# Kernel tuning notes

Hardware: AMD Instinct MI355X
Metric: run time of the kernel (lower is better)

The kernel has to match this reference:

```python
import jax, jax.numpy as jnp
import numpy as np
import math

D = 1024      # d_model
H = 16        # n_heads
DH = 64       # d_head
V = 32000     # vocab_size
MAXS = 2048   # max_seq_length
B, S = 2, 2048
PAD = 0
NEG = -1000000000.0
EPS = 1e-5


def _layernorm(x, g, b):
    mu = jnp.mean(x, axis=-1, keepdims=True)
    var = jnp.mean(jnp.square(x - mu), axis=-1, keepdims=True)
    return (x - mu) * jax.lax.rsqrt(var + EPS) * g + b


def _pad_mask(ids):
    # (b,1,1,S) additive mask over key columns where token == PAD
    return jnp.where((ids == PAD)[:, None, None, :], NEG, 0.0).astype(jnp.float32)


def _attn(Q, K, V_, out_w, out_b, causal_mask, pad_mask):
    # Q,K,V_: [b,n,s,d]
    logits = jnp.einsum('bnqd,bnkd->bnqk', Q, K) / math.sqrt(DH)
    if causal_mask is not None:
        logits = logits + causal_mask
    if pad_mask is not None:
        logits = logits + pad_mask
    probs = jax.nn.softmax(logits, axis=-1)
    o = jnp.einsum('bnqk,bnkd->bnqd', probs, V_)
    b, n, s, d = o.shape
    o = o.transpose(0, 2, 1, 3).reshape(b, s, n * d)  # b s (n d)
    return o @ out_w + out_b


def _heads(x, w, b):
    y = x @ w + b  # [b,s,H*DH]
    bs, s, _ = y.shape
    return y.reshape(bs, s, H, DH).transpose(0, 2, 1, 3)  # b n s d


def setup_inputs() -> dict:
    key = jax.random.key(0)
    ks = jax.random.split(key, 32)
    p = lambda i, shp, sc=0.02: (jax.random.normal(ks[i], shp, jnp.float32) * sc)
    inp = {
        'input_embedding': jax.random.normal(ks[0], (B, S, D), jnp.float32),
        'input_ids': jax.random.randint(ks[1], (B, S), 0, V),
        'target_ids': jax.random.randint(ks[2], (B, S), 0, V),
        'tok_emb': p(3, (V, D), 1.0),
        'pos_emb': p(4, (MAXS, D), 1.0),
        'ln1_g': jnp.ones((D,)), 'ln1_b': jnp.zeros((D,)),
        'q1_w': p(5, (D, H * DH)), 'q1_b': jnp.zeros((H * DH,)),
        'k1_w': p(6, (D, H * DH)), 'k1_b': jnp.zeros((H * DH,)),
        'v1_w': p(7, (D, H * DH)), 'v1_b': jnp.zeros((H * DH,)),
        'out1_w': p(8, (H * DH, D)), 'out1_b': jnp.zeros((D,)),
        'ln2_g': jnp.ones((D,)), 'ln2_b': jnp.zeros((D,)),
        'q2_w': p(9, (D, H * DH)), 'q2_b': jnp.zeros((H * DH,)),
        'k2_w': p(10, (D, H * DH)), 'k2_b': jnp.zeros((H * DH,)),
        'v2_w': p(11, (D, H * DH)), 'v2_b': jnp.zeros((H * DH,)),
        'out2_w': p(12, (H * DH, D)), 'out2_b': jnp.zeros((D,)),
        'ln3_g': jnp.ones((D,)), 'ln3_b': jnp.zeros((D,)),
        'mlp_w1': p(13, (D, 4 * D)), 'mlp_b1': jnp.zeros((4 * D,)),
        'mlp_w2': p(14, (4 * D, D)), 'mlp_b2': jnp.zeros((D,)),
    }
    return inp


def reference(input_embedding, input_ids, target_ids, tok_emb, pos_emb,
              ln1_g, ln1_b, q1_w, q1_b, k1_w, k1_b, v1_w, v1_b, out1_w, out1_b,
              ln2_g, ln2_b, q2_w, q2_b, k2_w, k2_b, v2_w, v2_b, out2_w, out2_b,
              ln3_g, ln3_b, mlp_w1, mlp_b1, mlp_w2, mlp_b2):
    b, s = target_ids.shape
    # embedding + positional
    x = tok_emb[target_ids] + pos_emb[jnp.arange(s)][None, :, :]
    x = _layernorm(x, ln1_g, ln1_b)
    # masked self-attention
    Q = _heads(x, q1_w, q1_b)
    K = _heads(x, k1_w, k1_b)
    Vv = _heads(x, v1_w, v1_b)
    causal = jnp.triu(jnp.full((s, s), NEG, jnp.float32), k=1)[None, None]
    attn = _attn(Q, K, Vv, out1_w, out1_b, causal, _pad_mask(target_ids))
    h = x + attn
    h = _layernorm(h, ln2_g, ln2_b)
    # cross-attention against encoder states
    Qc = _heads(h, q2_w, q2_b)
    Kc = _heads(input_embedding, k2_w, k2_b)
    Vc = _heads(input_embedding, v2_w, v2_b)
    cross = _attn(Qc, Kc, Vc, out2_w, out2_b, None, _pad_mask(input_ids))
    r = cross + h
    # MLP with exact GELU (torch nn.GELU default)
    z = _layernorm(r, ln3_g, ln3_b)
    mlp = jax.nn.gelu(z @ mlp_w1 + mlp_b1, approximate=False) @ mlp_w2 + mlp_b2
    return mlp + r
```

## Files before the change

kernel.cpp:

```cpp
#include <hip/hip_runtime.h>
#include <hip/hip_bf16.h>

#define S_LEN 2048
#define NEGF -1000000000.0f
#define QSC 0.18033688f

typedef unsigned short ushort_t;
typedef __attribute__((ext_vector_type(8))) short short8;
typedef __attribute__((ext_vector_type(4))) float f32x4;

#if defined(__has_builtin)
#if __has_builtin(__builtin_amdgcn_exp2f)
#define EXP2 __builtin_amdgcn_exp2f
#endif
#endif
#ifndef EXP2
#define EXP2 exp2f
#endif

__device__ __forceinline__ unsigned short f2b(float f) {
  unsigned int u = __float_as_uint(f);
  return (unsigned short)((u + 0x7fffu + ((u >> 16) & 1u)) >> 16);
}

__device__ __forceinline__ void gld_lds16(const void* g, void* l) {
  __builtin_amdgcn_global_load_lds((__attribute__((address_space(1))) unsigned int*)g,
                                   (__attribute__((address_space(3))) unsigned int*)l, 16, 0, 0);
}

__device__ __forceinline__ void wtrans_body(const float* __restrict__ W,
                                            ushort_t* __restrict__ Wt, int K, int N,
                                            int bx, int by) {
  __shared__ float t[32][33];
  int n0 = bx * 32, k0 = by * 32;
  int tx = threadIdx.x & 31, ty = threadIdx.x >> 5;
#pragma unroll
  for (int i = 0; i < 32; i += 8)
    t[ty + i][tx] = W[(size_t)(k0 + ty + i) * N + n0 + tx];
  __syncthreads();
#pragma unroll
  for (int i = 0; i < 32; i += 8)
    Wt[(size_t)(n0 + ty + i) * K + k0 + tx] = f2b(t[tx][ty + i]);
}

__global__ __launch_bounds__(256) void wtrans(const float* __restrict__ W,
                                              ushort_t* __restrict__ Wt, int K, int N) {
  wtrans_body(W, Wt, K, N, blockIdx.x, blockIdx.y);
}

struct P8 {
  const float* s[8];
  ushort_t* d[8];
};
__global__ __launch_bounds__(256) void wtrans8(P8 p) {
  wtrans_body(p.s[blockIdx.z], p.d[blockIdx.z], 1024, 1024, blockIdx.x, blockIdx.y);
}

__global__ __launch_bounds__(256) void f2bcvt(const float* __restrict__ in,
                                              ushort_t* __restrict__ out) {
  size_t i = ((size_t)blockIdx.x * 256 + threadIdx.x) * 4;
  float4 v = *(const float4*)(in + i);
  union { unsigned short u[4]; uint2 q; } pk;
  pk.u[0] = f2b(v.x); pk.u[1] = f2b(v.y); pk.u[2] = f2b(v.z); pk.u[3] = f2b(v.w);
  *(uint2*)(out + i) = pk.q;
}

__global__ __launch_bounds__(256) void bcat(float* __restrict__ dst, const float* __restrict__ a,
                                            const float* __restrict__ b,
                                            const float* __restrict__ c, int n0, int n1) {
  int i = blockIdx.x * 256 + threadIdx.x;
  float v = (i < n0) ? a[i] : (i < n0 + n1 ? b[i - n0] : c[i - n0 - n1]);
  dst[i] = v;
}

__global__ __launch_bounds__(256) void padmask(const int* __restrict__ tids,
                                               const int* __restrict__ iids,
                                               float* __restrict__ pmA,
                                               float* __restrict__ pmB) {
  int i = blockIdx.x * 256 + threadIdx.x;
  pmA[i] = (tids[i] == 0) ? NEGF : 0.0f;
  pmB[i] = (iids[i] == 0) ? NEGF : 0.0f;
}

__device__ __forceinline__ void row_stats(float s, float ss, float* outMean, float* outRstd) {
  __shared__ float red[8];
#pragma unroll
  for (int o = 32; o > 0; o >>= 1) {
    s += __shfl_down(s, o);
    ss += __shfl_down(ss, o);
  }
  int wave = threadIdx.x >> 6, lane = threadIdx.x & 63;
  if (lane == 0) { red[wave] = s; red[4 + wave] = ss; }
  __syncthreads();
  if (threadIdx.x == 0) {
    float S0 = red[0] + red[1] + red[2] + red[3];
    float S1 = red[4] + red[5] + red[6] + red[7];
    float mean = S0 * (1.0f / 1024.0f);
    float var = S1 * (1.0f / 1024.0f) - mean * mean;
    red[0] = mean;
    red[1] = rsqrtf(var + 1e-5f);
  }
  __syncthreads();
  *outMean = red[0];
  *outRstd = red[1];
}

__global__ __launch_bounds__(256) void embed_ln(const int* __restrict__ tids,
                                                const float* __restrict__ tok,
                                                const float* __restrict__ pos,
                                                const float* __restrict__ g,
                                                const float* __restrict__ be,
                                                float* __restrict__ xf,
                                                ushort_t* __restrict__ xb) {
  int row = blockIdx.x;
  int s = row & (S_LEN - 1);
  int id = tids[row];
  int c = threadIdx.x * 4;
  float4 v = *(const float4*)(tok + (size_t)id * 1024 + c);
  float4 p = *(const float4*)(pos + (size_t)s * 1024 + c);
  v.x += p.x; v.y += p.y; v.z += p.z; v.w += p.w;
  float mean, rstd;
  row_stats(v.x + v.y + v.z + v.w, v.x * v.x + v.y * v.y + v.z * v.z + v.w * v.w, &mean, &rstd);
  float4 gv = *(const float4*)(g + c);
  float4 bv = *(const float4*)(be + c);
  float4 o;
  o.x = (v.x - mean) * rstd * gv.x + bv.x;
  o.y = (v.y - mean) * rstd * gv.y + bv.y;
  o.z = (v.z - mean) * rstd * gv.z + bv.z;
  o.w = (v.w - mean) * rstd * gv.w + bv.w;
  *(float4*)(xf + (size_t)row * 1024 + c) = o;
  union { unsigned short u[4]; uint2 q; } pk;
  pk.u[0] = f2b(o.x); pk.u[1] = f2b(o.y); pk.u[2] = f2b(o.z); pk.u[3] = f2b(o.w);
  *(uint2*)(xb + (size_t)row * 1024 + c) = pk.q;
}

__global__ __launch_bounds__(256) void ln_fwd(const float* in, const float* __restrict__ g,
                                              const float* __restrict__ be, float* outF,
                                              ushort_t* __restrict__ outB) {
  int row = blockIdx.x;
  int c = threadIdx.x * 4;
  float4 v = *(const float4*)(in + (size_t)row * 1024 + c);
  float mean, rstd;
  row_stats(v.x + v.y + v.z + v.w, v.x * v.x + v.y * v.y + v.z * v.z + v.w * v.w, &mean, &rstd);
  float4 gv = *(const float4*)(g + c);
  float4 bv = *(const float4*)(be + c);
  float4 o;
  o.x = (v.x - mean) * rstd * gv.x + bv.x;
  o.y = (v.y - mean) * rstd * gv.y + bv.y;
  o.z = (v.z - mean) * rstd * gv.z + bv.z;
  o.w = (v.w - mean) * rstd * gv.w + bv.w;
  if (outF) *(float4*)(outF + (size_t)row * 1024 + c) = o;
  union { unsigned short u[4]; uint2 q; } pk;
  pk.u[0] = f2b(o.x); pk.u[1] = f2b(o.y); pk.u[2] = f2b(o.z); pk.u[3] = f2b(o.w);
  *(uint2*)(outB + (size_t)row * 1024 + c) = pk.q;
}

__global__ __launch_bounds__(256) void gemm_bt(const ushort_t* __restrict__ A,
                                               const ushort_t* __restrict__ Bt,
                                               const float* __restrict__ bias,
                                               const float* __restrict__ res,
                                               float* __restrict__ outF,
                                               ushort_t* __restrict__ outB,
                                               ushort_t* __restrict__ outT,
                                               int M, int N, int K, int act, int scaleN,
                                               int nSplit) {
  __shared__ __align__(16) ushort_t lA[128 * 64];
  __shared__ __align__(16) ushort_t lB[128 * 64];
  const int tid = threadIdx.x;
  const int wave = tid >> 6, lane = tid & 63;
  const int quad = lane >> 4, l16 = lane & 15;
  const int m0 = blockIdx.y * 128, n0 = blockIdx.x * 128;
  const int wm = (wave >> 1) * 64, wn = (wave & 1) * 64;

  f32x4 zero4 = {0.f, 0.f, 0.f, 0.f};
  f32x4 acc[4][4];
#pragma unroll
  for (int i = 0; i < 4; ++i)
#pragma unroll
    for (int j = 0; j < 4; ++j) acc[i][j] = zero4;

  int rowS[4], chkS[4];
#pragma unroll
  for (int ii = 0; ii < 4; ++ii) {
    int d = (wave * 4 + ii) * 64 + lane;
    rowS[ii] = d >> 3;
    chkS[ii] = (d & 7) ^ (rowS[ii] & 7);
  }

  for (int kt = 0; kt < K; kt += 64) {
    __syncthreads();
#pragma unroll
    for (int ii = 0; ii < 4; ++ii) {
      gld_lds16(A + (size_t)(m0 + rowS[ii]) * K + kt + chkS[ii] * 8,
                (char*)lA + (wave * 4 + ii) * 1024);
      gld_lds16(Bt + (size_t)(n0 + rowS[ii]) * K + kt + chkS[ii] * 8,
                (char*)lB + (wave * 4 + ii) * 1024);
    }
    __syncthreads();
#pragma unroll
    for (int kc = 0; kc < 2; ++kc) {
      short8 af[4], bf[4];
#pragma unroll
      for (int mt = 0; mt < 4; ++mt) {
        int r = wm + mt * 16 + l16;
        int c = (kc * 4 + quad) ^ (r & 7);
        af[mt] = *(const short8*)(lA + r * 64 + c * 8);
      }
#pragma unroll
      for (int nt = 0; nt < 4; ++nt) {
        int r = wn + nt * 16 + l16;
        int c = (kc * 4 + quad) ^ (r & 7);
        bf[nt] = *(const short8*)(lB + r * 64 + c * 8);
      }
#pragma unroll
      for (int mt = 0; mt < 4; ++mt)
#pragma unroll
        for (int nt = 0; nt < 4; ++nt)
          acc[mt][nt] = __builtin_amdgcn_mfma_f32_16x16x32_bf16(af[mt], bf[nt], acc[mt][nt], 0, 0, 0);
    }
  }

#pragma unroll
  for (int nt = 0; nt < 4; ++nt) {
    int gn = n0 + wn + nt * 16 + l16;
    float bv = bias[gn];
    if (gn < nSplit) {
#pragma unroll
      for (int mt = 0; mt < 4; ++mt) {
        int gmb = m0 + wm + mt * 16 + quad * 4;
#pragma unroll
        for (int reg = 0; reg < 4; ++reg) {
          size_t idx = (size_t)(gmb + reg) * nSplit + gn;
          float v = acc[mt][nt][reg] + bv;
          if (act == 1) v = 0.5f * v * (1.0f + erff(v * 0.70710678118654752f));
          if (gn < scaleN) v *= QSC;
          if (res) v += res[idx];
          if (outF) outF[idx] = v;
          if (outB) outB[idx] = f2b(v);
        }
      }
    } else {
#pragma unroll
      for (int mt = 0; mt < 4; ++mt) {
        int gmb = m0 + wm + mt * 16 + quad * 4;
        union { unsigned short u[4]; uint2 q; } pk;
#pragma unroll
        for (int reg = 0; reg < 4; ++reg) pk.u[reg] = f2b(acc[mt][nt][reg] + bv);
        *(uint2*)(outT + (size_t)(gn - nSplit) * M + gmb) = pk.q;
      }
    }
  }
}

__global__ __launch_bounds__(512, 2) void gemm256(const ushort_t* __restrict__ A,
                                                  const ushort_t* __restrict__ Bt,
                                                  const float* __restrict__ bias,
                                                  const float* __restrict__ res,
                                                  float* __restrict__ outF,
                                                  ushort_t* __restrict__ outB,
                                                  ushort_t* __restrict__ outT,
                                                  int M, int N, int K, int act, int scaleN,
                                                  int nSplit) {
  __shared__ __align__(16) ushort_t sA[2][256 * 64];
  __shared__ __align__(16) ushort_t sB[2][256 * 64];
  const int tid = threadIdx.x;
  const int wave = tid >> 6, lane = tid & 63;
  const int quad = lane >> 4, l16 = lane & 15;
  const int m0 = blockIdx.y * 256, n0 = blockIdx.x * 256;
  const int wm = (wave >> 2) * 128, wn = (wave & 3) * 64;

  const ushort_t* Ab = A + (size_t)m0 * K;
  const ushort_t* Bb = Bt + (size_t)n0 * K;

  const int srow = tid >> 3;
  const int schk = ((tid & 7) ^ (srow & 7)) << 3;

#define STAGE_H(SRC, LD, KT, DST, H)                                          \
  do {                                                                        \
    gld_lds16((SRC) + (size_t)((H) * 128 + srow) * (LD) + (KT) + schk,        \
              (char*)(DST) + (H) * 16384 + tid * 16);                         \
    gld_lds16((SRC) + (size_t)((H) * 128 + 64 + srow) * (LD) + (KT) + schk,   \
              (char*)(DST) + (H) * 16384 + 8192 + tid * 16);                  \
  } while (0)

  f32x4 zero4 = {0.f, 0.f, 0.f, 0.f};
  f32x4 acc[8][4];
#pragma unroll
  for (int i = 0; i < 8; ++i)
#pragma unroll
    for (int j = 0; j < 4; ++j) acc[i][j] = zero4;

  const int NT = K >> 6;

  STAGE_H(Ab, K, 0, sA[0], 0);
  STAGE_H(Ab, K, 0, sA[0], 1);
  STAGE_H(Bb, K, 0, sB[0], 0);
  STAGE_H(Bb, K, 0, sB[0], 1);
  asm volatile("s_waitcnt vmcnt(0)" ::: "memory");
  __builtin_amdgcn_s_barrier();

  for (int t = 0; t < NT; ++t) {
    const ushort_t* curA = sA[t & 1];
    const ushort_t* curB = sB[t & 1];
    ushort_t* nxtA = sA[(t + 1) & 1];
    ushort_t* nxtB = sB[(t + 1) & 1];
    const int ktn = (t + 1) << 6;
    const bool more = (t + 1 < NT);
#pragma unroll
    for (int q = 0; q < 4; ++q) {
      const int mh = q >> 1, nh = q & 1;
      short8 af[4][2], bf[2][2];
#pragma unroll
      for (int mt = 0; mt < 4; ++mt)
#pragma unroll
        for (int kc = 0; kc < 2; ++kc) {
          int r = wm + (mh * 4 + mt) * 16 + l16;
          af[mt][kc] = *(const short8*)(curA + r * 64 + (((kc * 4 + quad) ^ (r & 7)) << 3));
        }
#pragma unroll
      for (int nt = 0; nt < 2; ++nt)
#pragma unroll
        for (int kc = 0; kc < 2; ++kc) {
          int r = wn + (nh * 2 + nt) * 16 + l16;
          bf[nt][kc] = *(const short8*)(curB + r * 64 + (((kc * 4 + quad) ^ (r & 7)) << 3));
        }
      if (more) {
        if (q == 0) {
          STAGE_H(Ab, K, ktn, nxtA, 0);
          STAGE_H(Ab, K, ktn, nxtA, 1);
        } else if (q == 1) {
          STAGE_H(Bb, K, ktn, nxtB, 0);
          STAGE_H(Bb, K, ktn, nxtB, 1);
        }
      }
      __builtin_amdgcn_s_barrier();
      asm volatile("s_waitcnt lgkmcnt(0)" ::: "memory");
      __builtin_amdgcn_s_setprio(1);
#pragma unroll
      for (int mt = 0; mt < 4; ++mt)
#pragma unroll
        for (int nt = 0; nt < 2; ++nt)
#pragma unroll
          for (int kc = 0; kc < 2; ++kc)
            acc[mh * 4 + mt][nh * 2 + nt] = __builtin_amdgcn_mfma_f32_16x16x32_bf16(
                af[mt][kc], bf[nt][kc], acc[mh * 4 + mt][nh * 2 + nt], 0, 0, 0);
      __builtin_amdgcn_s_setprio(0);
      if (q == 3) asm volatile("s_waitcnt vmcnt(0)" ::: "memory");
      __builtin_amdgcn_s_barrier();
    }
  }
#undef STAGE_H

#pragma unroll
  for (int nt = 0; nt < 4; ++nt) {
    int gn = n0 + wn + nt * 16 + l16;
    float bv = bias[gn];
    if (gn < nSplit) {
#pragma unroll
      for (int mt = 0; mt < 8; ++mt) {
        int gmb = m0 + wm + mt * 16 + quad * 4;
#pragma unroll
        for (int reg = 0; reg < 4; ++reg) {
          size_t idx = (size_t)(gmb + reg) * nSplit + gn;
          float v = acc[mt][nt][reg] + bv;
          if (act == 1) v = 0.5f * v * (1.0f + erff(v * 0.70710678118654752f));
          if (gn < scaleN) v *= QSC;
          if (res) v += res[idx];
          if (outF) outF[idx] = v;
          if (outB) outB[idx] = f2b(v);
        }
      }
    } else {
#pragma unroll
      for (int mt = 0; mt < 8; ++mt) {
        int gmb = m0 + wm + mt * 16 + quad * 4;
        union { unsigned short u[4]; uint2 q2; } pk;
#pragma unroll
        for (int reg = 0; reg < 4; ++reg) pk.u[reg] = f2b(acc[mt][nt][reg] + bv);
        *(uint2*)(outT + (size_t)(gn - nSplit) * M + gmb) = pk.q2;
      }
    }
  }
}

__global__ __launch_bounds__(256) void gemm_n64(const ushort_t* __restrict__ A,
                                                const ushort_t* __restrict__ Bt,
                                                const float* __restrict__ bias,
                                                const float* __restrict__ res,
                                                float* __restrict__ outF,
                                                ushort_t* __restrict__ outB,
                                                int M, int N, int K, int act, int scaleN) {
  __shared__ __align__(16) ushort_t lA[2][128 * 64];
  __shared__ __align__(16) ushort_t lB[2][64 * 64];
  const int tid = threadIdx.x;
  const int wave = tid >> 6, lane = tid & 63;
  const int quad = lane >> 4, l16 = lane & 15;
  const int m0 = blockIdx.y * 128, n0 = blockIdx.x * 64;
  const int wm = wave * 32;

  f32x4 zero4 = {0.f, 0.f, 0.f, 0.f};
  f32x4 acc[2][4];
#pragma unroll
  for (int i = 0; i < 2; ++i)
#pragma unroll
    for (int j = 0; j < 4; ++j) acc[i][j] = zero4;

  int rowA[4], chkA[4], rowB[2], chkB[2];
#pragma unroll
  for (int ii = 0; ii < 4; ++ii) {
    int d = (wave * 4 + ii) * 64 + lane;
    rowA[ii] = d >> 3;
    chkA[ii] = (d & 7) ^ (rowA[ii] & 7);
  }
#pragma unroll
  for (int ii = 0; ii < 2; ++ii) {
    int d = (wave * 2 + ii) * 64 + lane;
    rowB[ii] = d >> 3;
    chkB[ii] = (d & 7) ^ (rowB[ii] & 7);
  }

#define STG64(KT, BUF)                                                         \
  do {                                                                         \
    _Pragma("unroll") for (int ii = 0; ii < 4; ++ii)                           \
        gld_lds16(A + (size_t)(m0 + rowA[ii]) * K + (KT) + chkA[ii] * 8,       \
                  (char*)lA[BUF] + (wave * 4 + ii) * 1024);                    \
    _Pragma("unroll") for (int ii = 0; ii < 2; ++ii)                           \
        gld_lds16(Bt + (size_t)(n0 + rowB[ii]) * K + (KT) + chkB[ii] * 8,      \
                  (char*)lB[BUF] + (wave * 2 + ii) * 1024);                    \
  } while (0)

  STG64(0, 0);
  __syncthreads();

  int cur = 0;
  for (int kt = 0; kt < K; kt += 64) {
    if (kt + 64 < K) STG64(kt + 64, cur ^ 1);
    const ushort_t* cA = lA[cur];
    const ushort_t* cB = lB[cur];
#pragma unroll
    for (int kc = 0; kc < 2; ++kc) {
      short8 af[2], bf[4];
#pragma unroll
      for (int mt = 0; mt < 2; ++mt) {
        int r = wm + mt * 16 + l16;
        int c = (kc * 4 + quad) ^ (r & 7);
        af[mt] = *(const short8*)(cA + r * 64 + c * 8);
      }
#pragma unroll
      for (int nt = 0; nt < 4; ++nt) {
        int r = nt * 16 + l16;
        int c = (kc * 4 + quad) ^ (r & 7);
        bf[nt] = *(const short8*)(cB + r * 64 + c * 8);
      }
#pragma unroll
      for (int mt = 0; mt < 2; ++mt)
#pragma unroll
        for (int nt = 0; nt < 4; ++nt)
          acc[mt][nt] = __builtin_amdgcn_mfma_f32_16x16x32_bf16(af[mt], bf[nt], acc[mt][nt], 0, 0, 0);
    }
    __syncthreads();
    cur ^= 1;
  }
#undef STG64

#pragma unroll
  for (int nt = 0; nt < 4; ++nt) {
    int gn = n0 + nt * 16 + l16;
    float bv = bias[gn];
#pragma unroll
    for (int mt = 0; mt < 2; ++mt) {
      int gmb = m0 + wm + mt * 16 + quad * 4;
#pragma unroll
      for (int reg = 0; reg < 4; ++reg) {
        size_t idx = (size_t)(gmb + reg) * N + gn;
        float v = acc[mt][nt][reg] + bv;
        if (act == 1) v = 0.5f * v * (1.0f + erff(v * 0.70710678118654752f));
        if (gn < scaleN) v *= QSC;
        if (res) v += res[idx];
        if (outF) outF[idx] = v;
        if (outB) outB[idx] = f2b(v);
      }
    }
  }
}

template <int CAUSAL>
__global__ __launch_bounds__(256, 4) void attn4(const ushort_t* __restrict__ Qp, int ldQ,
                                                const ushort_t* __restrict__ Kp, int ldK,
                                                const ushort_t* __restrict__ Vt,
                                                const float* __restrict__ pmg,
                                                ushort_t* __restrict__ O) {
  __shared__ __align__(16) ushort_t lK[2][64 * 64];
  __shared__ __align__(16) ushort_t lV[2][64 * 64];
  __shared__ __align__(16) ushort_t lP[4][16 * 64];

  const int h = blockIdx.y, b = blockIdx.z;
  const int g = CAUSAL ? (31 - (int)blockIdx.x) : (int)blockIdx.x;
  const int tid = threadIdx.x;
  const int wave = tid >> 6, lane = tid & 63;
  const int quad = lane >> 4, l16 = lane & 15;
  const int g0 = g * 64;
  const float* pmb = pmg + b * S_LEN;

  const int qrow = g0 + wave * 16 + l16;
  const ushort_t* qb = Qp + ((size_t)(b * S_LEN) + qrow) * ldQ + h * 64;
  short8 qf[2];
  qf[0] = *(const short8*)(qb + quad * 8);
  qf[1] = *(const short8*)(qb + 32 + quad * 8);

  f32x4 zero4 = {0.f, 0.f, 0.f, 0.f};
  f32x4 acc_o[4];
#pragma unroll
  for (int nt = 0; nt < 4; ++nt) acc_o[nt] = zero4;
  float lsum[4] = {0.f, 0.f, 0.f, 0.f};

  const int nkv = CAUSAL ? (g + 1) : (S_LEN / 64);
  const int qbase = g0 + wave * 16 + quad * 4;

  int srow[2], scs[2];
#pragma unroll
  for (int ii = 0; ii < 2; ++ii) {
    int slot = (wave * 2 + ii) * 64 + lane;
    srow[ii] = slot >> 3;
    scs[ii] = ((slot & 7) ^ (srow[ii] & 7)) * 8;
  }

#define STAGE_KV(KV0, BUF)                                                            \
  do {                                                                                \
    _Pragma("unroll") for (int ii = 0; ii < 2; ++ii) {                                \
      gld_lds16(Kp + (size_t)(b * S_LEN + (KV0) + srow[ii]) * ldK + h * 64 + scs[ii], \
                (char*)lK[BUF] + (wave * 2 + ii) * 1024);                             \
      gld_lds16(Vt + (size_t)(h * 64 + srow[ii]) * 4096 + b * S_LEN + (KV0) + scs[ii],\
                (char*)lV[BUF] + (wave * 2 + ii) * 1024);                             \
    }                                                                                 \
  } while (0)

  STAGE_KV(0, 0);
  __syncthreads();

  int cur = 0;
  for (int kv = 0; kv < nkv; ++kv) {
    const int kv0 = kv * 64;
    if (kv + 1 < nkv) STAGE_KV(kv0 + 64, cur ^ 1);

    float pmv[4];
#pragma unroll
    for (int nt = 0; nt < 4; ++nt) pmv[nt] = pmb[kv0 + nt * 16 + l16];

    const ushort_t* cK = lK[cur];
    const ushort_t* cV = lV[cur];

    f32x4 sacc[4];
#pragma unroll
    for (int nt = 0; nt < 4; ++nt) sacc[nt] = zero4;
#pragma unroll
    for (int kc = 0; kc < 2; ++kc) {
#pragma unroll
      for (int nt = 0; nt < 4; ++nt) {
        int r = nt * 16 + l16;
        int c = (kc * 4 + quad) ^ (r & 7);
        short8 kf = *(const short8*)(cK + r * 64 + c * 8);
        sacc[nt] = __builtin_amdgcn_mfma_f32_16x16x32_bf16(qf[kc], kf, sacc[nt], 0, 0, 0);
      }
    }

    const bool diag = CAUSAL && (kv == g);
#pragma unroll
    for (int nt = 0; nt < 4; ++nt) {
      int kk = kv0 + nt * 16 + l16;
#pragma unroll
      for (int reg = 0; reg < 4; ++reg) {
        float s = sacc[nt][reg] + pmv[nt];
        if (diag && kk > qbase + reg) s = NEGF;
        float p = EXP2(s);
        lsum[reg] += p;
        int q = quad * 4 + reg;
        int cc = (nt * 2 + (l16 >> 3)) ^ (q & 7);
        lP[wave][q * 64 + cc * 8 + (l16 & 7)] = f2b(p);
      }
    }

#pragma unroll
    for (int kc = 0; kc < 2; ++kc) {
      int cp = (kc * 4 + quad) ^ (l16 & 7);
      short8 pf = *(const short8*)(&lP[wave][l16 * 64 + cp * 8]);
#pragma unroll
      for (int nt = 0; nt < 4; ++nt) {
        int r = nt * 16 + l16;
        int c = (kc * 4 + quad) ^ (r & 7);
        short8 vf = *(const short8*)(cV + r * 64 + c * 8);
        acc_o[nt] = __builtin_amdgcn_mfma_f32_16x16x32_bf16(pf, vf, acc_o[nt], 0, 0, 0);
      }
    }
    __syncthreads();
    cur ^= 1;
  }
#undef STAGE_KV

  float inv[4];
#pragma unroll
  for (int reg = 0; reg < 4; ++reg) {
    float t = lsum[reg];
    t += __shfl_xor(t, 1);
    t += __shfl_xor(t, 2);
    t += __shfl_xor(t, 4);
    t += __shfl_xor(t, 8);
    inv[reg] = 1.0f / t;
  }
#pragma unroll
  for (int nt = 0; nt < 4; ++nt)
#pragma unroll
    for (int reg = 0; reg < 4; ++reg) {
      int qr = g0 + wave * 16 + quad * 4 + reg;
      O[((size_t)(b * S_LEN) + qr) * 1024 + h * 64 + nt * 16 + l16] =
          f2b(acc_o[nt][reg] * inv[reg]);
    }
}

extern "C" void kernel_launch(void* const* d_in, const int* in_sizes, int n_in,
                              void* d_out, int out_size, void* d_ws, size_t ws_size,
                              hipStream_t stream) {
  (void)in_sizes; (void)n_in; (void)out_size; (void)ws_size;
  const size_t MB = 1024 * 1024;
  char* w = (char*)d_ws;
  ushort_t* qkv1T = (ushort_t*)(w + 0);
  ushort_t* o1T = (ushort_t*)(w + 6 * MB);
  ushort_t* q2T = (ushort_t*)(w + 8 * MB);
  ushort_t* k2v2T = (ushort_t*)(w + 10 * MB);
  ushort_t* o2T = (ushort_t*)(w + 14 * MB);
  ushort_t* m1T = (ushort_t*)(w + 16 * MB);
  ushort_t* m2T = (ushort_t*)(w + 24 * MB);
  float* bias3 = (float*)(w + 32 * MB);
  float* bias2 = (float*)(w + 32 * MB + 64 * 1024);
  float* pmA = (float*)(w + 32 * MB + 128 * 1024);
  float* pmB = (float*)(w + 32 * MB + 160 * 1024);
  ushort_t* xb = (ushort_t*)(w + 33 * MB);
  ushort_t* QKb = (ushort_t*)(w + 41 * MB);
  ushort_t* Vt = (ushort_t*)(w + 57 * MB);
  ushort_t* Ob = (ushort_t*)(w + 65 * MB);
  ushort_t* encb = (ushort_t*)(w + 73 * MB);
  float* xf = (float*)(w + 81 * MB);
  float* hf = (float*)(w + 97 * MB);
  ushort_t* m1b = (ushort_t*)(w + 113 * MB);
  ushort_t* hlnb = xb;
  ushort_t* Q2b = QKb;
  ushort_t* K2b = QKb + 4 * MB;

  dim3 B256(256);
  dim3 B512(512);
  P8 p8;
  p8.s[0] = (const float*)d_in[7];  p8.d[0] = qkv1T;
  p8.s[1] = (const float*)d_in[9];  p8.d[1] = qkv1T + 1024 * 1024;
  p8.s[2] = (const float*)d_in[11]; p8.d[2] = qkv1T + 2 * 1024 * 1024;
  p8.s[3] = (const float*)d_in[13]; p8.d[3] = o1T;
  p8.s[4] = (const float*)d_in[17]; p8.d[4] = q2T;
  p8.s[5] = (const float*)d_in[19]; p8.d[5] = k2v2T;
  p8.s[6] = (const float*)d_in[21]; p8.d[6] = k2v2T + 1024 * 1024;
  p8.s[7] = (const float*)d_in[23]; p8.d[7] = o2T;
  wtrans8<<<dim3(32, 32, 8), B256, 0, stream>>>(p8);
  wtrans<<<dim3(128, 32), B256, 0, stream>>>((const float*)d_in[27], m1T, 1024, 4096);
  wtrans<<<dim3(32, 128), B256, 0, stream>>>((const float*)d_in[29], m2T, 4096, 1024);
  f2bcvt<<<4096, B256, 0, stream>>>((const float*)d_in[0], encb);
  bcat<<<12, B256, 0, stream>>>(bias3, (const float*)d_in[8], (const float*)d_in[10],
                                (const float*)d_in[12], 1024, 1024);
  bcat<<<8, B256, 0, stream>>>(bias2, (const float*)d_in[20], (const float*)d_in[22],
                               (const float*)d_in[22], 1024, 1024);
  padmask<<<16, B256, 0, stream>>>((const int*)d_in[2], (const int*)d_in[1], pmA, pmB);

  embed_ln<<<4096, B256, 0, stream>>>((const int*)d_in[2], (const float*)d_in[3],
                                      (const float*)d_in[4], (const float*)d_in[5],
                                      (const float*)d_in[6], xf, xb);
  gemm_bt<<<dim3(24, 32), B256, 0, stream>>>(xb, qkv1T, bias3, nullptr, nullptr, QKb, Vt,
                                             4096, 3072, 1024, 0, 1024, 2048);
  attn4<1><<<dim3(32, 16, 2), B256, 0, stream>>>(QKb, 2048, QKb + 1024, 2048, Vt, pmA, Ob);
  gemm_n64<<<dim3(16, 32), B256, 0, stream>>>(Ob, o1T, (const float*)d_in[14], xf, hf, nullptr,
                                              4096, 1024, 1024, 0, 0);
  ln_fwd<<<4096, B256, 0, stream>>>(hf, (const float*)d_in[15], (const float*)d_in[16], hf, hlnb);
  gemm_n64<<<dim3(16, 32), B256, 0, stream>>>(hlnb, q2T, (const float*)d_in[18], nullptr, nullptr,
                                              Q2b, 4096, 1024, 1024, 0, 1024);
  gemm_bt<<<dim3(16, 32), B256, 0, stream>>>(encb, k2v2T, bias2, nullptr, nullptr, K2b, Vt,
                                             4096, 2048, 1024, 0, 0, 1024);
  attn4<0><<<dim3(32, 16, 2), B256, 0, stream>>>(Q2b, 1024, K2b, 1024, Vt, pmB, Ob);
  gemm_n64<<<dim3(16, 32), B256, 0, stream>>>(Ob, o2T, (const float*)d_in[24], hf, xf, nullptr,
                                              4096, 1024, 1024, 0, 0);
  ln_fwd<<<4096, B256, 0, stream>>>(xf, (const float*)d_in[25], (const float*)d_in[26], nullptr,
                                    hlnb);
  gemm256<<<dim3(16, 16), B512, 0, stream>>>(hlnb, m1T, (const float*)d_in[28], nullptr, nullptr,
                                             m1b, nullptr, 4096, 4096, 1024, 1, 0, 4096);
  gemm_n64<<<dim3(16, 32), B256, 0, stream>>>(m1b, m2T, (const float*)d_in[30], xf, (float*)d_out,
                                              nullptr, 4096, 1024, 4096, 0, 0);
}
```

Baseline: 710.0 us.

## Rework gemm256 schedule, single-buffer gemm_n64, and double query rows in attention

The 256-wide GEMM main loop now issues all next-tile global-to-LDS loads up front and runs a snake-ordered sequence of fragment loads and MFMAs, so fragments are reused across quadrants and per-quadrant barriers are dropped. gemm_n64 moves from double-buffered LDS to a single buffer with two barriers per K step, which halves its LDS footprint but exposes load latency. The attention kernel now handles 128 query rows per block (two 64-row sub-tiles) so each K/V tile loaded into LDS and registers is reused twice, at the cost of more registers and lower occupancy (launch bound 2).

```diff
diff --git a/kernel.cpp b/kernel.cpp
--- a/kernel.cpp
+++ b/kernel.cpp
@@ -293,11 +293,36 @@
   const int NT = K >> 6;
 
   STAGE_H(Ab, K, 0, sA[0], 0);
-  STAGE_H(Ab, K, 0, sA[0], 1);
   STAGE_H(Bb, K, 0, sB[0], 0);
   STAGE_H(Bb, K, 0, sB[0], 1);
+  STAGE_H(Ab, K, 0, sA[0], 1);
   asm volatile("s_waitcnt vmcnt(0)" ::: "memory");
   __builtin_amdgcn_s_barrier();
+
+#define LDA(MH)                                                                     \
+  do {                                                                              \
+    _Pragma("unroll") for (int mt = 0; mt < 4; ++mt)                                \
+        _Pragma("unroll") for (int kc = 0; kc < 2; ++kc) {                          \
+      int r = wm + ((MH) * 4 + mt) * 16 + l16;                                      \
+      af[mt][kc] = *(const short8*)(curA + r * 64 + (((kc * 4 + quad) ^ (r & 7)) << 3)); \
+    }                                                                               \
+  } while (0)
+#define LDB(NH)                                                                     \
+  do {                                                                              \
+    _Pragma("unroll") for (int nt = 0; nt < 2; ++nt)                                \
+        _Pragma("unroll") for (int kc = 0; kc < 2; ++kc) {                          \
+      int r = wn + ((NH) * 2 + nt) * 16 + l16;                                      \
+      bf[nt][kc] = *(const short8*)(curB + r * 64 + (((kc * 4 + quad) ^ (r & 7)) << 3)); \
+    }                                                                               \
+  } while (0)
+#define FMA(MH, NH)                                                                 \
+  do {                                                                              \
+    _Pragma("unroll") for (int kc = 0; kc < 2; ++kc)                                \
+        _Pragma("unroll") for (int mt = 0; mt < 4; ++mt)                            \
+            _Pragma("unroll") for (int nt = 0; nt < 2; ++nt)                        \
+        acc[(MH) * 4 + mt][(NH) * 2 + nt] = __builtin_amdgcn_mfma_f32_16x16x32_bf16( \
+            af[mt][kc], bf[nt][kc], acc[(MH) * 4 + mt][(NH) * 2 + nt], 0, 0, 0);    \
+  } while (0)
 
   for (int t = 0; t < NT; ++t) {
     const ushort_t* curA = sA[t & 1];
@@ -305,51 +330,28 @@
     ushort_t* nxtA = sA[(t + 1) & 1];
     ushort_t* nxtB = sB[(t + 1) & 1];
     const int ktn = (t + 1) << 6;
-    const bool more = (t + 1 < NT);
-#pragma unroll
-    for (int q = 0; q < 4; ++q) {
-      const int mh = q >> 1, nh = q & 1;
-      short8 af[4][2], bf[2][2];
-#pragma unroll
-      for (int mt = 0; mt < 4; ++mt)
-#pragma unroll
-        for (int kc = 0; kc < 2; ++kc) {
-          int r = wm + (mh * 4 + mt) * 16 + l16;
-          af[mt][kc] = *(const short8*)(curA + r * 64 + (((kc * 4 + quad) ^ (r & 7)) << 3));
-        }
-#pragma unroll
-      for (int nt = 0; nt < 2; ++nt)
-#pragma unroll
-        for (int kc = 0; kc < 2; ++kc) {
-          int r = wn + (nh * 2 + nt) * 16 + l16;
-          bf[nt][kc] = *(const short8*)(curB + r * 64 + (((kc * 4 + quad) ^ (r & 7)) << 3));
-        }
-      if (more) {
-        if (q == 0) {
-          STAGE_H(Ab, K, ktn, nxtA, 0);
-          STAGE_H(Ab, K, ktn, nxtA, 1);
-        } else if (q == 1) {
-          STAGE_H(Bb, K, ktn, nxtB, 0);
-          STAGE_H(Bb, K, ktn, nxtB, 1);
-        }
-      }
-      __builtin_amdgcn_s_barrier();
-      asm volatile("s_waitcnt lgkmcnt(0)" ::: "memory");
-      __builtin_amdgcn_s_setprio(1);
-#pragma unroll
-      for (int mt = 0; mt < 4; ++mt)
-#pragma unroll
-        for (int nt = 0; nt < 2; ++nt)
-#pragma unroll
-          for (int kc = 0; kc < 2; ++kc)
-            acc[mh * 4 + mt][nh * 2 + nt] = __builtin_amdgcn_mfma_f32_16x16x32_bf16(
-                af[mt][kc], bf[nt][kc], acc[mh * 4 + mt][nh * 2 + nt], 0, 0, 0);
-      __builtin_amdgcn_s_setprio(0);
-      if (q == 3) asm volatile("s_waitcnt vmcnt(0)" ::: "memory");
-      __builtin_amdgcn_s_barrier();
-    }
+    if (t + 1 < NT) {
+      STAGE_H(Ab, K, ktn, nxtA, 0);
+      STAGE_H(Bb, K, ktn, nxtB, 0);
+      STAGE_H(Bb, K, ktn, nxtB, 1);
+      STAGE_H(Ab, K, ktn, nxtA, 1);
+    }
+    short8 af[4][2], bf[2][2];
+    LDA(0); LDB(0);
+    FMA(0, 0);
+    LDB(1);
+    FMA(0, 1);
+    LDA(1);
+    FMA(1, 1);
+    LDB(0);
+    FMA(1, 0);
+    asm volatile("s_waitcnt vmcnt(0)" ::: "memory");
+    __builtin_amdgcn_s_barrier();
   }
 #undef STAGE_H
+#undef LDA
+#undef LDB
+#undef FMA
 
 #pragma unroll
   for (int nt = 0; nt < 4; ++nt) {
@@ -390,8 +392,8 @@
                                                 float* __restrict__ outF,
                                                 ushort_t* __restrict__ outB,
                                                 int M, int N, int K, int act, int scaleN) {
-  __shared__ __align__(16) ushort_t lA[2][128 * 64];
-  __shared__ __align__(16) ushort_t lB[2][64 * 64];
+  __shared__ __align__(16) ushort_t lA[128 * 64];
+  __shared__ __align__(16) ushort_t lB[64 * 64];
   const int tid = threadIdx.x;
   const int wave = tid >> 6, lane = tid & 63;
   const int quad = lane >> 4, l16 = lane & 15;
@@ -419,24 +421,17 @@
     chkB[ii] = (d & 7) ^ (rowB[ii] & 7);
   }
 
-#define STG64(KT, BUF)                                                         \
-  do {                                                                         \
-    _Pragma("unroll") for (int ii = 0; ii < 4; ++ii)                           \
-        gld_lds16(A + (size_t)(m0 + rowA[ii]) * K + (KT) + chkA[ii] * 8,       \
-                  (char*)lA[BUF] + (wave * 4 + ii) * 1024);                    \
-    _Pragma("unroll") for (int ii = 0; ii < 2; ++ii)                           \
-        gld_lds16(Bt + (size_t)(n0 + rowB[ii]) * K + (KT) + chkB[ii] * 8,      \
-                  (char*)lB[BUF] + (wave * 2 + ii) * 1024);                    \
-  } while (0)
-
-  STG64(0, 0);
-  __syncthreads();
-
-  int cur = 0;
   for (int kt = 0; kt < K; kt += 64) {
-    if (kt + 64 < K) STG64(kt + 64, cur ^ 1);
-    const ushort_t* cA = lA[cur];
-    const ushort_t* cB = lB[cur];
+    __syncthreads();
+#pragma unroll
+    for (int ii = 0; ii < 4; ++ii)
+      gld_lds16(A + (size_t)(m0 + rowA[ii]) * K + kt + chkA[ii] * 8,
+                (char*)lA + (wave * 4 + ii) * 1024);
+#pragma unroll
+    for (int ii = 0; ii < 2; ++ii)
+      gld_lds16(Bt + (size_t)(n0 + rowB[ii]) * K + kt + chkB[ii] * 8,
+                (char*)lB + (wave * 2 + ii) * 1024);
+    __syncthreads();
 #pragma unroll
     for (int kc = 0; kc < 2; ++kc) {
       short8 af[2], bf[4];
@@ -444,13 +439,13 @@
       for (int mt = 0; mt < 2; ++mt) {
         int r = wm + mt * 16 + l16;
         int c = (kc * 4 + quad) ^ (r & 7);
-        af[mt] = *(const short8*)(cA + r * 64 + c * 8);
+        af[mt] = *(const short8*)(lA + r * 64 + c * 8);
       }
 #pragma unroll
       for (int nt = 0; nt < 4; ++nt) {
         int r = nt * 16 + l16;
         int c = (kc * 4 + quad) ^ (r & 7);
-        bf[nt] = *(const short8*)(cB + r * 64 + c * 8);
+        bf[nt] = *(const short8*)(lB + r * 64 + c * 8);
       }
 #pragma unroll
       for (int mt = 0; mt < 2; ++mt)
@@ -458,10 +453,7 @@
         for (int nt = 0; nt < 4; ++nt)
           acc[mt][nt] = __builtin_amdgcn_mfma_f32_16x16x32_bf16(af[mt], bf[nt], acc[mt][nt], 0, 0, 0);
     }
-    __syncthreads();
-    cur ^= 1;
-  }
-#undef STG64
+  }
 
 #pragma unroll
   for (int nt = 0; nt < 4; ++nt) {
@@ -485,7 +477,7 @@
 }
 
 template <int CAUSAL>
-__global__ __launch_bounds__(256, 4) void attn4(const ushort_t* __restrict__ Qp, int ldQ,
+__global__ __launch_bounds__(256, 2) void attn5(const ushort_t* __restrict__ Qp, int ldQ,
                                                 const ushort_t* __restrict__ Kp, int ldK,
                                                 const ushort_t* __restrict__ Vt,
                                                 const float* __restrict__ pmg,
@@ -495,27 +487,34 @@
   __shared__ __align__(16) ushort_t lP[4][16 * 64];
 
   const int h = blockIdx.y, b = blockIdx.z;
-  const int g = CAUSAL ? (31 - (int)blockIdx.x) : (int)blockIdx.x;
+  const int g = CAUSAL ? (15 - (int)blockIdx.x) : (int)blockIdx.x;
   const int tid = threadIdx.x;
   const int wave = tid >> 6, lane = tid & 63;
   const int quad = lane >> 4, l16 = lane & 15;
-  const int g0 = g * 64;
+  const int g0 = g * 128;
   const float* pmb = pmg + b * S_LEN;
 
-  const int qrow = g0 + wave * 16 + l16;
-  const ushort_t* qb = Qp + ((size_t)(b * S_LEN) + qrow) * ldQ + h * 64;
-  short8 qf[2];
-  qf[0] = *(const short8*)(qb + quad * 8);
-  qf[1] = *(const short8*)(qb + 32 + quad * 8);
+  short8 qf[2][2];
+#pragma unroll
+  for (int s = 0; s < 2; ++s) {
+    const ushort_t* qb =
+        Qp + ((size_t)(b * S_LEN) + g0 + s * 64 + wave * 16 + l16) * ldQ + h * 64;
+    qf[s][0] = *(const short8*)(qb + quad * 8);
+    qf[s][1] = *(const short8*)(qb + 32 + quad * 8);
+  }
 
   f32x4 zero4 = {0.f, 0.f, 0.f, 0.f};
-  f32x4 acc_o[4];
-#pragma unroll
-  for (int nt = 0; nt < 4; ++nt) acc_o[nt] = zero4;
-  float lsum[4] = {0.f, 0.f, 0.f, 0.f};
-
-  const int nkv = CAUSAL ? (g + 1) : (S_LEN / 64);
-  const int qbase = g0 + wave * 16 + quad * 4;
+  f32x4 acc_o[2][4];
+  float lsum[2][4];
+#pragma unroll
+  for (int s = 0; s < 2; ++s)
+#pragma unroll
+    for (int nt = 0; nt < 4; ++nt) {
+      acc_o[s][nt] = zero4;
+      lsum[s][nt] = 0.f;
+    }
+
+  const int nkv = CAUSAL ? (2 * g + 2) : (S_LEN / 64);
 
   int srow[2], scs[2];
 #pragma unroll
@@ -550,46 +549,54 @@
     const ushort_t* cK = lK[cur];
     const ushort_t* cV = lV[cur];
 
-    f32x4 sacc[4];
-#pragma unroll
-    for (int nt = 0; nt < 4; ++nt) sacc[nt] = zero4;
-#pragma unroll
-    for (int kc = 0; kc < 2; ++kc) {
+    short8 kf[2][4], vf[2][4];
+#pragma unroll
+    for (int kc = 0; kc < 2; ++kc)
 #pragma unroll
       for (int nt = 0; nt < 4; ++nt) {
         int r = nt * 16 + l16;
         int c = (kc * 4 + quad) ^ (r & 7);
-        short8 kf = *(const short8*)(cK + r * 64 + c * 8);
-        sacc[nt] = __builtin_amdgcn_mfma_f32_16x16x32_bf16(qf[kc], kf, sacc[nt], 0, 0, 0);
-      }
-    }
-
-    const bool diag = CAUSAL && (kv == g);
-#pragma unroll
-    for (int nt = 0; nt < 4; ++nt) {
-      int kk = kv0 + nt * 16 + l16;
-#pragma unroll
-      for (int reg = 0; reg < 4; ++reg) {
-        float s = sacc[nt][reg] + pmv[nt];
-        if (diag && kk > qbase + reg) s = NEGF;
-        float p = EXP2(s);
-        lsum[reg] += p;
-        int q = quad * 4 + reg;
-        int cc = (nt * 2 + (l16 >> 3)) ^ (q & 7);
-        lP[wave][q * 64 + cc * 8 + (l16 & 7)] = f2b(p);
-      }
-    }
-
-#pragma unroll
-    for (int kc = 0; kc < 2; ++kc) {
-      int cp = (kc * 4 + quad) ^ (l16 & 7);
-      short8 pf = *(const short8*)(&lP[wave][l16 * 64 + cp * 8]);
+        kf[kc][nt] = *(const short8*)(cK + r * 64 + c * 8);
+        vf[kc][nt] = *(const short8*)(cV + r * 64 + c * 8);
+      }
+
+#pragma unroll
+    for (int s = 0; s < 2; ++s) {
+      if (CAUSAL && kv > 2 * g + s) continue;
+
+      f32x4 sacc[4];
+#pragma unroll
+      for (int nt = 0; nt < 4; ++nt) sacc[nt] = zero4;
+#pragma unroll
+      for (int kc = 0; kc < 2; ++kc)
+#pragma unroll
+        for (int nt = 0; nt < 4; ++nt)
+          sacc[nt] = __builtin_amdgcn_mfma_f32_16x16x32_bf16(qf[s][kc], kf[kc][nt], sacc[nt], 0, 0, 0);
+
+      const int qbase = g0 + s * 64 + wave * 16 + quad * 4;
+      const bool diag = CAUSAL && (kv == 2 * g + s);
 #pragma unroll
       for (int nt = 0; nt < 4; ++nt) {
-        int r = nt * 16 + l16;
-        int c = (kc * 4 + quad) ^ (r & 7);
-        short8 vf = *(const short8*)(cV + r * 64 + c * 8);
-        acc_o[nt] = __builtin_amdgcn_mfma_f32_16x16x32_bf16(pf, vf, acc_o[nt], 0, 0, 0);
+        int kk = kv0 + nt * 16 + l16;
+#pragma unroll
+        for (int reg = 0; reg < 4; ++reg) {
+          float sv = sacc[nt][reg] + pmv[nt];
+          if (diag && kk > qbase + reg) sv = NEGF;
+          float p = EXP2(sv);
+          lsum[s][reg] += p;
+          int q = quad * 4 + reg;
+          int cc = (nt * 2 + (l16 >> 3)) ^ (q & 7);
+          lP[wave][q * 64 + cc * 8 + (l16 & 7)] = f2b(p);
+        }
+      }
+
+#pragma unroll
+      for (int kc = 0; kc < 2; ++kc) {
+        int cp = (kc * 4 + quad) ^ (l16 & 7);
+        short8 pf = *(const short8*)(&lP[wave][l16 * 64 + cp * 8]);
+#pragma unroll
+        for (int nt = 0; nt < 4; ++nt)
+          acc_o[s][nt] = __builtin_amdgcn_mfma_f32_16x16x32_bf16(pf, vf[kc][nt], acc_o[s][nt], 0, 0, 0);
       }
     }
     __syncthreads();
@@ -597,24 +604,27 @@
   }
 #undef STAGE_KV
 
-  float inv[4];
-#pragma unroll
-  for (int reg = 0; reg < 4; ++reg) {
-    float t = lsum[reg];
-    t += __shfl_xor(t, 1);
-    t += __shfl_xor(t, 2);
-    t += __shfl_xor(t, 4);
-    t += __shfl_xor(t, 8);
-    inv[reg] = 1.0f / t;
-  }
-#pragma unroll
-  for (int nt = 0; nt < 4; ++nt)
+#pragma unroll
+  for (int s = 0; s < 2; ++s) {
+    float inv[4];
 #pragma unroll
     for (int reg = 0; reg < 4; ++reg) {
-      int qr = g0 + wave * 16 + quad * 4 + reg;
-      O[((size_t)(b * S_LEN) + qr) * 1024 + h * 64 + nt * 16 + l16] =
-          f2b(acc_o[nt][reg] * inv[reg]);
-    }
+      float t = lsum[s][reg];
+      t += __shfl_xor(t, 1);
+      t += __shfl_xor(t, 2);
+      t += __shfl_xor(t, 4);
+      t += __shfl_xor(t, 8);
+      inv[reg] = 1.0f / t;
+    }
+#pragma unroll
+    for (int nt = 0; nt < 4; ++nt)
+#pragma unroll
+      for (int reg = 0; reg < 4; ++reg) {
+        int qr = g0 + s * 64 + wave * 16 + quad * 4 + reg;
+        O[((size_t)(b * S_LEN) + qr) * 1024 + h * 64 + nt * 16 + l16] =
+            f2b(acc_o[s][nt][reg] * inv[reg]);
+      }
+  }
 }
 
 extern "C" void kernel_launch(void* const* d_in, const int* in_sizes, int n_in,
@@ -672,7 +682,7 @@
                                       (const float*)d_in[6], xf, xb);
   gemm_bt<<<dim3(24, 32), B256, 0, stream>>>(xb, qkv1T, bias3, nullptr, nullptr, QKb, Vt,
                                              4096, 3072, 1024, 0, 1024, 2048);
-  attn4<1><<<dim3(32, 16, 2), B256, 0, stream>>>(QKb, 2048, QKb + 1024, 2048, Vt, pmA, Ob);
+  attn5<1><<<dim3(16, 16, 2), B256, 0, stream>>>(QKb, 2048, QKb + 1024, 2048, Vt, pmA, Ob);
   gemm_n64<<<dim3(16, 32), B256, 0, stream>>>(Ob, o1T, (const float*)d_in[14], xf, hf, nullptr,
                                               4096, 1024, 1024, 0, 0);
   ln_fwd<<<4096, B256, 0, stream>>>(hf, (const float*)d_in[15], (const float*)d_in[16], hf, hlnb);
@@ -680,7 +690,7 @@
                                               Q2b, 4096, 1024, 1024, 0, 1024);
   gemm_bt<<<dim3(16, 32), B256, 0, stream>>>(encb, k2v2T, bias2, nullptr, nullptr, K2b, Vt,
                                              4096, 2048, 1024, 0, 0, 1024);
-  attn4<0><<<dim3(32, 16, 2), B256, 0, stream>>>(Q2b, 1024, K2b, 1024, Vt, pmB, Ob);
+  attn5<0><<<dim3(16, 16, 2), B256, 0, stream>>>(Q2b, 1024, K2b, 1024, Vt, pmB, Ob);
   gemm_n64<<<dim3(16, 32), B256, 0, stream>>>(Ob, o2T, (const float*)d_in[24], hf, xf, nullptr,
                                               4096, 1024, 1024, 0, 0);
   ln_fwd<<<4096, B256, 0, stream>>>(xf, (const float*)d_in[25], (const float*)d_in[26], nullptr,
```

New measurement: 708.5 us. Within noise of the previous version (-0.2%).
